# Optimization experiments

Measured on AMD Instinct MI355X. Metric: run time of the kernel, lower is better.

Reference implementation:

```python
import jax, jax.numpy as jnp
import numpy as np

D_MODEL = 1024
N_INPUT = 4096
N_PROCESS = 2048
D_ROUTING = 256
TEMPERATURE = 0.5
LN_EPS = 1e-5


def _gelu(x):
    return jax.nn.gelu(x, approximate=False)  # torch F.gelu default (erf)


def setup_inputs() -> dict:
    key = jax.random.key(0)
    ks = jax.random.split(key, 10)
    B, S = 8, 2048
    x = jax.random.normal(ks[0], (B, S, D_MODEL), dtype=jnp.float32)
    # GlobalRouter query_net: Linear(d_model, 2*d_routing) -> GELU -> LayerNorm -> Linear(2*d_routing, d_routing)
    W1 = jax.random.normal(ks[1], (2 * D_ROUTING, D_MODEL), dtype=jnp.float32) * (2.0 / (D_MODEL + 2 * D_ROUTING)) ** 0.5 * 1.414
    b1 = jnp.zeros((2 * D_ROUTING,), dtype=jnp.float32)
    ln_g = jnp.ones((2 * D_ROUTING,), dtype=jnp.float32)
    ln_b = jnp.zeros((2 * D_ROUTING,), dtype=jnp.float32)
    W2 = jax.random.normal(ks[2], (D_ROUTING, 2 * D_ROUTING), dtype=jnp.float32) * (2.0 / (3 * D_ROUTING)) ** 0.5 * 1.414
    b2 = jnp.zeros((D_ROUTING,), dtype=jnp.float32)
    neuron_keys = jax.random.normal(ks[3], (N_INPUT, D_ROUTING), dtype=jnp.float32) / D_ROUTING ** 0.5 * 1.414
    input_patterns = jax.random.normal(ks[4], (N_INPUT, D_MODEL), dtype=jnp.float32) / D_MODEL ** 0.5 * 1.414
    process_weights = jax.random.normal(ks[5], (N_PROCESS, N_INPUT), dtype=jnp.float32) / N_INPUT ** 0.5 * 1.414
    process_outputs = jax.random.normal(ks[6], (N_PROCESS, D_MODEL), dtype=jnp.float32) / D_MODEL ** 0.5 * 1.414
    return {
        'x': x, 'k_input': 2048, 'k_process': 1024,
        'W1': W1, 'b1': b1, 'ln_g': ln_g, 'ln_b': ln_b, 'W2': W2, 'b2': b2,
        'neuron_keys': neuron_keys, 'input_patterns': input_patterns,
        'process_weights': process_weights, 'process_outputs': process_outputs,
    }


def _forward(x, k_input, k_process, W1, b1, ln_g, ln_b, W2, b2,
             neuron_keys, input_patterns, process_weights, process_outputs):
    B, S, d_model = x.shape
    # ---- GlobalRouter ----
    gctx = jnp.max(x, axis=1)                                  # [B, d_model]
    h = _gelu(gctx @ W1.T + b1)                                # [B, 2*d_routing]
    mu = jnp.mean(h, axis=-1, keepdims=True)
    var = jnp.mean((h - mu) ** 2, axis=-1, keepdims=True)
    h = (h - mu) * jax.lax.rsqrt(var + LN_EPS) * ln_g + ln_b
    query = h @ W2.T + b2                                      # [B, d_routing]
    logits = (query @ neuron_keys.T) / D_ROUTING ** 0.5        # [B, n_input]
    probs = jax.nn.softmax(logits / TEMPERATURE, axis=-1)
    _, input_idx = jax.lax.top_k(logits, k_input)              # [B, k_input]
    one_hot = jnp.zeros_like(probs).at[jnp.arange(B)[:, None], input_idx].set(1.0)
    routing_weights = jax.lax.stop_gradient(one_hot - probs) + probs  # STE
    # ---- input neuron stage ----
    input_acts = _gelu(jnp.einsum('bsd,nd->bsn', x, input_patterns))   # [B,S,n_input]
    weighted = input_acts * routing_weights[:, None, :]
    sel_in = jnp.take_along_axis(weighted, input_idx[:, None, :], axis=2)  # [B,S,k_input]
    # gather process weight columns per batch: [B, n_process, k_input]
    W_sel = jnp.transpose(process_weights[:, input_idx], (1, 0, 2))
    process_acts = _gelu(jnp.einsum('bsk,bpk->bsp', sel_in, W_sel))    # [B,S,n_process]
    # ---- process neuron stage ----
    process_scores = jnp.mean(process_acts, axis=1)                    # [B,n_process]
    _, process_idx = jax.lax.top_k(process_scores, k_process)          # [B,k_process]
    sel_proc = jnp.take_along_axis(process_acts, process_idx[:, None, :], axis=2)  # [B,S,k_process]
    out_sel = process_outputs[process_idx]                             # [B,k_process,d_model]
    return jnp.einsum('bsp,bpd->bsd', sel_proc, out_sel)


def reference(x, k_input, k_process, W1, b1, ln_g, ln_b, W2, b2,
              neuron_keys, input_patterns, process_weights, process_outputs):
    return _forward(x, k_input, k_process, W1, b1, ln_g, ln_b, W2, b2,
                    neuron_keys, input_patterns, process_weights, process_outputs)
```

## Files before the change

kernel.cpp:

```cpp
#include <hip/hip_runtime.h>
#include <stdint.h>

#define B_  8
#define S_  2048
#define DM  1024
#define NI  4096
#define NP  2048
#define DR  256
#define H2  512
#define KI  2048
#define KP  1024
#define LDW 40

typedef __attribute__((ext_vector_type(8))) short bf16x8;
typedef __attribute__((ext_vector_type(4))) float f32x4;
typedef unsigned short ushort;
typedef unsigned int uint;

__device__ __forceinline__ float gelu_erf(float v){
    return 0.5f * v * (1.0f + erff(v * 0.7071067811865476f));
}
__device__ __forceinline__ ushort f2b(float f){
    union { float f; uint u; } a; a.f = f;
    uint r = a.u + 0x7fffu + ((a.u >> 16) & 1u);
    return (ushort)(r >> 16);
}
__device__ __forceinline__ float b2f(ushort u){
    union { uint u; float f; } a; a.u = ((uint)u) << 16; return a.f;
}
__device__ __forceinline__ void cvt8(const float* p, uint4& H, uint4& L){
    uint h[4], l[4];
    #pragma unroll
    for(int i = 0; i < 4; i++){
        ushort h0 = f2b(p[2*i]);   float f0 = b2f(h0); ushort l0 = f2b(p[2*i]   - f0);
        ushort h1 = f2b(p[2*i+1]); float f1 = b2f(h1); ushort l1 = f2b(p[2*i+1] - f1);
        h[i] = (uint)h0 | ((uint)h1 << 16);
        l[i] = (uint)l0 | ((uint)l1 << 16);
    }
    H = uint4{h[0],h[1],h[2],h[3]};
    L = uint4{l[0],l[1],l[2],l[3]};
}
__device__ __forceinline__ void gload_lds16(const void* g, void* l){
    __builtin_amdgcn_global_load_lds((const __attribute__((address_space(1))) void*)g,
                                     (__attribute__((address_space(3))) void*)l, 16, 0, 0);
}

__global__ __launch_bounds__(256) void k_pre(const float* __restrict__ x,
                                             const float* __restrict__ patt,
                                             const float* __restrict__ pout,
                                             float* __restrict__ gpart,
                                             ushort* __restrict__ xh,
                                             ushort* __restrict__ xl,
                                             ushort* __restrict__ patth,
                                             ushort* __restrict__ pattl,
                                             ushort* __restrict__ poutb){
    int bid = blockIdx.x;
    int t = threadIdx.x;
    if(bid < 512){
        int b = bid >> 6, ch = bid & 63;
        size_t row0 = (size_t)b*S_ + (size_t)ch*32;
        const float4* xb = (const float4*)(x + row0*DM);
        float4 m = float4{-3.402823466e38f, -3.402823466e38f, -3.402823466e38f, -3.402823466e38f};
        for(int r = 0; r < 32; r++){
            float4 v = xb[(size_t)r*(DM/4) + t];
            ushort hx = f2b(v.x), hy = f2b(v.y), hz = f2b(v.z), hw = f2b(v.w);
            uint2 H{ (uint)hx | ((uint)hy << 16), (uint)hz | ((uint)hw << 16) };
            uint2 L{ (uint)f2b(v.x - b2f(hx)) | ((uint)f2b(v.y - b2f(hy)) << 16),
                     (uint)f2b(v.z - b2f(hz)) | ((uint)f2b(v.w - b2f(hw)) << 16) };
            ((uint2*)(xh + (row0 + r)*DM))[t] = H;
            ((uint2*)(xl + (row0 + r)*DM))[t] = L;
            m.x = fmaxf(m.x, v.x); m.y = fmaxf(m.y, v.y);
            m.z = fmaxf(m.z, v.z); m.w = fmaxf(m.w, v.w);
        }
        ((float4*)(gpart + (size_t)(b*64 + ch)*DM))[t] = m;
    }else if(bid < 2560){
        size_t idx = (size_t)(bid - 512)*256 + t;
        float f[8];
        *(float4*)(f)     = ((const float4*)patt)[idx*2];
        *(float4*)(f + 4) = ((const float4*)patt)[idx*2 + 1];
        uint4 H, L; cvt8(f, H, L);
        ((uint4*)patth)[idx] = H;
        ((uint4*)pattl)[idx] = L;
    }else{
        size_t idx = (size_t)(bid - 2560)*256 + t;
        float f[8];
        *(float4*)(f)     = ((const float4*)pout)[idx*2];
        *(float4*)(f + 4) = ((const float4*)pout)[idx*2 + 1];
        uint o[4];
        #pragma unroll
        for(int i = 0; i < 4; i++)
            o[i] = (uint)f2b(f[2*i]) | ((uint)f2b(f[2*i+1]) << 16);
        ((uint4*)poutb)[idx] = uint4{o[0], o[1], o[2], o[3]};
    }
}

__global__ __launch_bounds__(256) void k_h(const float* __restrict__ gpart,
                                           const float* __restrict__ W1,
                                           const float* __restrict__ b1,
                                           float* __restrict__ h){
    __shared__ float g[DM];
    int b = blockIdx.x >> 3, ig = blockIdx.x & 7;
    int t = threadIdx.x;
    for(int d = t; d < DM; d += 256){
        float m = gpart[(size_t)(b*64)*DM + d];
        for(int c = 1; c < 64; c++) m = fmaxf(m, gpart[(size_t)(b*64 + c)*DM + d]);
        g[d] = m;
    }
    __syncthreads();
    int i  = ig*64 + (t >> 2);
    int dq = (t & 3) * 256;
    const float* wr = W1 + (size_t)i*DM + dq;
    const float* gg = g + dq;
    float s = 0.f;
    for(int d = 0; d < 256; d++) s = fmaf(gg[d], wr[d], s);
    s += __shfl_xor(s, 1);
    s += __shfl_xor(s, 2);
    if((t & 3) == 0) h[b*H2 + i] = gelu_erf(s + b1[i]);
}

__global__ __launch_bounds__(256) void k_query(const float* __restrict__ h,
                                               const float* __restrict__ lng,
                                               const float* __restrict__ lnb,
                                               const float* __restrict__ W2,
                                               const float* __restrict__ b2,
                                               float* __restrict__ query){
    __shared__ float hn[H2];
    __shared__ float red[4];
    int b = blockIdx.x >> 2, qg = blockIdx.x & 3;
    int t = threadIdx.x;
    float v0 = h[b*H2 + t], v1 = h[b*H2 + 256 + t];
    float s = v0 + v1;
    for(int o = 32; o > 0; o >>= 1) s += __shfl_down(s, o);
    if((t & 63) == 0) red[t >> 6] = s;
    __syncthreads();
    float mean = (red[0] + red[1] + red[2] + red[3]) * (1.f/H2);
    __syncthreads();
    float d0 = v0 - mean, d1 = v1 - mean;
    float sq = d0*d0 + d1*d1;
    for(int o = 32; o > 0; o >>= 1) sq += __shfl_down(sq, o);
    if((t & 63) == 0) red[t >> 6] = sq;
    __syncthreads();
    float var  = (red[0] + red[1] + red[2] + red[3]) * (1.f/H2);
    float rstd = rsqrtf(var + 1e-5f);
    hn[t]       = d0*rstd*lng[t]       + lnb[t];
    hn[256 + t] = d1*rstd*lng[256 + t] + lnb[256 + t];
    __syncthreads();
    int q  = qg*64 + (t >> 2);
    int iq = (t & 3) * 128;
    const float* wr = W2 + (size_t)q*H2 + iq;
    float acc = 0.f;
    for(int i2 = 0; i2 < 128; i2++) acc = fmaf(hn[iq + i2], wr[i2], acc);
    acc += __shfl_xor(acc, 1);
    acc += __shfl_xor(acc, 2);
    if((t & 3) == 0) query[b*DR + q] = acc + b2[q];
}

__global__ __launch_bounds__(256) void k_logits(const float* __restrict__ query,
                                                const float* __restrict__ nk,
                                                float* __restrict__ logits){
    __shared__ float4 q4[DR/4];
    int b = blockIdx.x >> 4, ng = blockIdx.x & 15;
    int t = threadIdx.x;
    if(t < 64) q4[t] = ((const float4*)(query + (size_t)b*DR))[t];
    __syncthreads();
    int w = t >> 6, lane = t & 63;
    float4 qv = q4[lane];
    int nbase = ng*256 + w*64;
    #pragma unroll 2
    for(int i = 0; i < 64; i++){
        int n = nbase + i;
        float4 v = ((const float4*)(nk + (size_t)n*DR))[lane];
        float p = v.x*qv.x + v.y*qv.y + v.z*qv.z + v.w*qv.w;
        p += __shfl_down(p, 32); p += __shfl_down(p, 16); p += __shfl_down(p, 8);
        p += __shfl_down(p, 4);  p += __shfl_down(p, 2);  p += __shfl_down(p, 1);
        if(lane == 0) logits[(size_t)b*NI + n] = p * 0.0625f;
    }
}

template<int N_, int KSEL>
__global__ __launch_bounds__(256) void k_topk(const float* __restrict__ vals,
                                              int* __restrict__ idxout){
    __shared__ unsigned u[N_];
    __shared__ int redc[4];
    __shared__ int sc[256];
    int t = threadIdx.x;
    size_t vbase = (size_t)blockIdx.x * N_;
    size_t obase = (size_t)blockIdx.x * KSEL;
    for(int i = t; i < N_; i += 256){
        unsigned bits = __float_as_uint(vals[vbase + i]);
        u[i] = (bits & 0x80000000u) ? ~bits : (bits | 0x80000000u);
    }
    __syncthreads();
    unsigned lo = 0u, hi = 0xFFFFFFFFu;
    while(lo < hi){
        unsigned mid = lo + (unsigned)((((unsigned long long)(hi - lo)) + 1ull) >> 1);
        int c = 0;
        for(int i = t; i < N_; i += 256) c += (u[i] >= mid) ? 1 : 0;
        for(int o = 32; o > 0; o >>= 1) c += __shfl_down(c, o);
        if((t & 63) == 0) redc[t >> 6] = c;
        __syncthreads();
        int tot = redc[0] + redc[1] + redc[2] + redc[3];
        if(tot >= KSEL) lo = mid; else hi = mid - 1;
        __syncthreads();
    }
    unsigned T = lo;
    const int PER = N_ / 256;
    int base = t * PER;
    int lgt = 0, leq = 0;
    for(int j = 0; j < PER; j++){
        unsigned v = u[base + j];
        lgt += (v > T) ? 1 : 0; leq += (v == T) ? 1 : 0;
    }
    sc[t] = (lgt << 16) | leq;
    __syncthreads();
    for(int o = 1; o < 256; o <<= 1){
        int add = (t >= o) ? sc[t - o] : 0;
        __syncthreads();
        sc[t] += add;
        __syncthreads();
    }
    int need = KSEL - (sc[255] >> 16);
    int ex = (t == 0) ? 0 : sc[t - 1];
    int pos = (ex >> 16) + ((ex & 0xffff) < need ? (ex & 0xffff) : need);
    int eq = ex & 0xffff;
    for(int j = 0; j < PER; j++){
        unsigned v = u[base + j];
        if(v > T){ idxout[obase + pos++] = base + j; }
        else if(v == T){ if(eq < need){ idxout[obase + pos++] = base + j; } eq++; }
    }
}

__global__ __launch_bounds__(256) void k_gemm1(const ushort* __restrict__ xh,
                                               const ushort* __restrict__ xl,
                                               const ushort* __restrict__ ph,
                                               const ushort* __restrict__ pl,
                                               const int* __restrict__ iidx,
                                               ushort* __restrict__ selh,
                                               ushort* __restrict__ sell, int b0){
    __shared__ __align__(16) ushort Ah[2][128*32], Al[2][128*32], Bh[2][128*32], Bl[2][128*32];
    __shared__ int rowmap[128];
    int t = threadIdx.x;
    int g = blockIdx.x >> 8, rest = blockIdx.x & 255;
    int b = b0 + g;
    int mb = rest >> 4, nb = rest & 15;
    int m0 = mb*128, n0 = nb*128;
    ushort* selh_g = selh + (size_t)g*S_*KI;
    ushort* sell_g = sell + (size_t)g*S_*KI;
    if(t < 128) rowmap[t] = iidx[(size_t)b*KI + n0 + t];
    __syncthreads();
    int w = t >> 6, l = t & 63;
    int lr = l >> 2, lc = l & 3;
    int r0 = 32*w + lr, r1 = r0 + 16;
    const ushort* pAh0 = xh + ((size_t)b*S_ + m0 + r0)*DM + lc*8;
    const ushort* pAh1 = xh + ((size_t)b*S_ + m0 + r1)*DM + lc*8;
    const ushort* pAl0 = xl + ((size_t)b*S_ + m0 + r0)*DM + lc*8;
    const ushort* pAl1 = xl + ((size_t)b*S_ + m0 + r1)*DM + lc*8;
    const ushort* pBh0 = ph + (size_t)rowmap[r0]*DM + lc*8;
    const ushort* pBh1 = ph + (size_t)rowmap[r1]*DM + lc*8;
    const ushort* pBl0 = pl + (size_t)rowmap[r0]*DM + lc*8;
    const ushort* pBl1 = pl + (size_t)rowmap[r1]*DM + lc*8;
    int d0 = w*1024, d1 = d0 + 512;
    #define STG1(BUF, KO) do{ \
        gload_lds16(pAh0 + (KO), &Ah[BUF][d0]); \
        gload_lds16(pAh1 + (KO), &Ah[BUF][d1]); \
        gload_lds16(pAl0 + (KO), &Al[BUF][d0]); \
        gload_lds16(pAl1 + (KO), &Al[BUF][d1]); \
        gload_lds16(pBh0 + (KO), &Bh[BUF][d0]); \
        gload_lds16(pBh1 + (KO), &Bh[BUF][d1]); \
        gload_lds16(pBl0 + (KO), &Bl[BUF][d0]); \
        gload_lds16(pBl1 + (KO), &Bl[BUF][d1]); \
    }while(0)
    STG1(0, 0);
    int lm = l & 15, q = l >> 4;
    int mbase = (w >> 1)*64, nbase = (w & 1)*64;
    f32x4 acc[4][4];
    #pragma unroll
    for(int i = 0; i < 4; i++)
      #pragma unroll
      for(int j = 0; j < 4; j++) acc[i][j] = f32x4{0.f,0.f,0.f,0.f};
    int cur = 0;
    for(int k0 = 0; k0 < DM; k0 += 32){
        if(k0 + 32 < DM){
            STG1(cur^1, k0 + 32);
            asm volatile("s_waitcnt vmcnt(8)" ::: "memory");
        }else{
            asm volatile("s_waitcnt vmcnt(0)" ::: "memory");
        }
        __builtin_amdgcn_s_barrier();
        asm volatile("" ::: "memory");
        bf16x8 ahf[4], alf[4];
        #pragma unroll
        for(int mt = 0; mt < 4; mt++){
            ahf[mt] = *(const bf16x8*)(&Ah[cur][(mbase + mt*16 + lm)*32 + q*8]);
            alf[mt] = *(const bf16x8*)(&Al[cur][(mbase + mt*16 + lm)*32 + q*8]);
        }
        __builtin_amdgcn_s_setprio(1);
        #pragma unroll
        for(int nt = 0; nt < 4; nt++){
            bf16x8 bhf = *(const bf16x8*)(&Bh[cur][(nbase + nt*16 + lm)*32 + q*8]);
            bf16x8 blf = *(const bf16x8*)(&Bl[cur][(nbase + nt*16 + lm)*32 + q*8]);
            #pragma unroll
            for(int mt = 0; mt < 4; mt++){
                acc[mt][nt] = __builtin_amdgcn_mfma_f32_16x16x32_bf16(ahf[mt], bhf, acc[mt][nt], 0, 0, 0);
                acc[mt][nt] = __builtin_amdgcn_mfma_f32_16x16x32_bf16(ahf[mt], blf, acc[mt][nt], 0, 0, 0);
                acc[mt][nt] = __builtin_amdgcn_mfma_f32_16x16x32_bf16(alf[mt], bhf, acc[mt][nt], 0, 0, 0);
            }
        }
        __builtin_amdgcn_s_setprio(0);
        asm volatile("s_waitcnt lgkmcnt(0)" ::: "memory");
        __builtin_amdgcn_s_barrier();
        asm volatile("" ::: "memory");
        cur ^= 1;
    }
    #undef STG1
    #pragma unroll
    for(int mt = 0; mt < 4; mt++)
      #pragma unroll
      for(int nt = 0; nt < 4; nt++){
        int col = n0 + nbase + nt*16 + lm;
        #pragma unroll
        for(int i = 0; i < 4; i++){
            int row = m0 + mbase + mt*16 + q*4 + i;
            float gv = gelu_erf(acc[mt][nt][i]);
            ushort hbits = f2b(gv);
            selh_g[(size_t)row*KI + col] = hbits;
            sell_g[(size_t)row*KI + col] = f2b(gv - b2f(hbits));
        }
      }
}

__global__ __launch_bounds__(256) void k_gather_wsel(const float* __restrict__ pw,
                                                     const int* __restrict__ iidx,
                                                     ushort* __restrict__ wh,
                                                     ushort* __restrict__ wl,
                                                     float* __restrict__ scores, int b0){
    int g = blockIdx.x >> 8, pc = blockIdx.x & 255;
    int b = b0 + g;
    ushort* wh_g = wh + (size_t)g*NP*KI;
    ushort* wl_g = wl + (size_t)g*NP*KI;
    int t = threadIdx.x;
    if(t < 8) scores[(size_t)b*NP + pc*8 + t] = 0.f;
    int j0 = t*8;
    int k8[8];
    *(int4*)(k8)     = *(const int4*)(iidx + (size_t)b*KI + j0);
    *(int4*)(k8 + 4) = *(const int4*)(iidx + (size_t)b*KI + j0 + 4);
    for(int r2 = 0; r2 < 8; r2++){
        int p = pc*8 + r2;
        const float* row = pw + (size_t)p*NI;
        uint hh[4], ll[4];
        #pragma unroll
        for(int i = 0; i < 4; i++){
            float v0 = row[k8[2*i]], v1 = row[k8[2*i+1]];
            ushort h0 = f2b(v0), h1 = f2b(v1);
            hh[i] = (uint)h0 | ((uint)h1 << 16);
            ll[i] = (uint)f2b(v0 - b2f(h0)) | ((uint)f2b(v1 - b2f(h1)) << 16);
        }
        *(uint4*)(wh_g + (size_t)p*KI + j0) = uint4{hh[0],hh[1],hh[2],hh[3]};
        *(uint4*)(wl_g + (size_t)p*KI + j0) = uint4{ll[0],ll[1],ll[2],ll[3]};
    }
}

__global__ __launch_bounds__(256) void k_gemm2(const ushort* __restrict__ selh,
                                               const ushort* __restrict__ sell,
                                               const ushort* __restrict__ wh,
                                               const ushort* __restrict__ wl,
                                               ushort* __restrict__ acts,
                                               float* __restrict__ scores, int b0){
    __shared__ __align__(16) ushort Ah[2][128*32], Al[2][128*32], Bh[2][128*32], Bl[2][128*32];
    __shared__ float colsum[128];
    int t = threadIdx.x;
    int g = blockIdx.x >> 8, rest = blockIdx.x & 255;
    int b = b0 + g;
    int mb = rest >> 4, nb = rest & 15;
    int m0 = mb*128, n0 = nb*128;
    const ushort* selh_g = selh + (size_t)g*S_*KI;
    const ushort* sell_g = sell + (size_t)g*S_*KI;
    const ushort* wh_g   = wh   + (size_t)g*NP*KI;
    const ushort* wl_g   = wl   + (size_t)g*NP*KI;
    ushort* acts_g = acts + (size_t)g*S_*NP;
    int w = t >> 6, l = t & 63;
    int lr = l >> 2, lc = l & 3;
    int r0 = 32*w + lr, r1 = r0 + 16;
    const ushort* pAh0 = selh_g + (size_t)(m0 + r0)*KI + lc*8;
    const ushort* pAh1 = selh_g + (size_t)(m0 + r1)*KI + lc*8;
    const ushort* pAl0 = sell_g + (size_t)(m0 + r0)*KI + lc*8;
    const ushort* pAl1 = sell_g + (size_t)(m0 + r1)*KI + lc*8;
    const ushort* pBh0 = wh_g + (size_t)(n0 + r0)*KI + lc*8;
    const ushort* pBh1 = wh_g + (size_t)(n0 + r1)*KI + lc*8;
    const ushort* pBl0 = wl_g + (size_t)(n0 + r0)*KI + lc*8;
    const ushort* pBl1 = wl_g + (size_t)(n0 + r1)*KI + lc*8;
    int d0 = w*1024, d1 = d0 + 512;
    #define STG2(BUF, KO) do{ \
        gload_lds16(pAh0 + (KO), &Ah[BUF][d0]); \
        gload_lds16(pAh1 + (KO), &Ah[BUF][d1]); \
        gload_lds16(pAl0 + (KO), &Al[BUF][d0]); \
        gload_lds16(pAl1 + (KO), &Al[BUF][d1]); \
        gload_lds16(pBh0 + (KO), &Bh[BUF][d0]); \
        gload_lds16(pBh1 + (KO), &Bh[BUF][d1]); \
        gload_lds16(pBl0 + (KO), &Bl[BUF][d0]); \
        gload_lds16(pBl1 + (KO), &Bl[BUF][d1]); \
    }while(0)
    STG2(0, 0);
    int lm = l & 15, q = l >> 4;
    int mbase = (w >> 1)*64, nbase = (w & 1)*64;
    f32x4 acc[4][4];
    #pragma unroll
    for(int i = 0; i < 4; i++)
      #pragma unroll
      for(int j = 0; j < 4; j++) acc[i][j] = f32x4{0.f,0.f,0.f,0.f};
    int cur = 0;
    for(int k0 = 0; k0 < KI; k0 += 32){
        if(k0 + 32 < KI){
            STG2(cur^1, k0 + 32);
            asm volatile("s_waitcnt vmcnt(8)" ::: "memory");
        }else{
            asm volatile("s_waitcnt vmcnt(0)" ::: "memory");
        }
        __builtin_amdgcn_s_barrier();
        asm volatile("" ::: "memory");
        bf16x8 ahf[4], alf[4];
        #pragma unroll
        for(int mt = 0; mt < 4; mt++){
            ahf[mt] = *(const bf16x8*)(&Ah[cur][(mbase + mt*16 + lm)*32 + q*8]);
            alf[mt] = *(const bf16x8*)(&Al[cur][(mbase + mt*16 + lm)*32 + q*8]);
        }
        __builtin_amdgcn_s_setprio(1);
        #pragma unroll
        for(int nt = 0; nt < 4; nt++){
            bf16x8 bhf = *(const bf16x8*)(&Bh[cur][(nbase + nt*16 + lm)*32 + q*8]);
            bf16x8 blf = *(const bf16x8*)(&Bl[cur][(nbase + nt*16 + lm)*32 + q*8]);
            #pragma unroll
            for(int mt = 0; mt < 4; mt++){
                acc[mt][nt] = __builtin_amdgcn_mfma_f32_16x16x32_bf16(ahf[mt], bhf, acc[mt][nt], 0, 0, 0);
                acc[mt][nt] = __builtin_amdgcn_mfma_f32_16x16x32_bf16(ahf[mt], blf, acc[mt][nt], 0, 0, 0);
                acc[mt][nt] = __builtin_amdgcn_mfma_f32_16x16x32_bf16(alf[mt], bhf, acc[mt][nt], 0, 0, 0);
            }
        }
        __builtin_amdgcn_s_setprio(0);
        asm volatile("s_waitcnt lgkmcnt(0)" ::: "memory");
        __builtin_amdgcn_s_barrier();
        asm volatile("" ::: "memory");
        cur ^= 1;
    }
    #undef STG2
    if(t < 128) colsum[t] = 0.f;
    __syncthreads();
    #pragma unroll
    for(int mt = 0; mt < 4; mt++)
      #pragma unroll
      for(int nt = 0; nt < 4; nt++){
        int cb = nbase + nt*16 + lm;
        float s4 = 0.f;
        #pragma unroll
        for(int i = 0; i < 4; i++){
            int row = m0 + mbase + mt*16 + q*4 + i;
            float gv = gelu_erf(acc[mt][nt][i]);
            s4 += gv;
            acts_g[(size_t)row*NP + n0 + cb] = f2b(gv);
        }
        atomicAdd(&colsum[cb], s4);
      }
    __syncthreads();
    if(t < 128) atomicAdd(&scores[(size_t)b*NP + n0 + t], colsum[t]);
}

__global__ __launch_bounds__(256) void k_gather_selacts(const ushort* __restrict__ acts,
                                                        const int* __restrict__ pidx,
                                                        ushort* __restrict__ selacts, int b0){
    int g = blockIdx.x >> 6, sc_ = blockIdx.x & 63;
    int b = b0 + g;
    const ushort* acts_g = acts + (size_t)g*S_*NP;
    ushort* selacts_g = selacts + (size_t)g*S_*KP;
    int t = threadIdx.x;
    int j0 = t*4;
    int4 p4 = *(const int4*)(pidx + (size_t)b*KP + j0);
    const ushort* Ab = acts_g    + ((size_t)sc_*32)*NP;
    ushort*       Ob = selacts_g + ((size_t)sc_*32)*KP;
    for(int r2 = 0; r2 < 32; r2++){
        const ushort* Ar = Ab + (size_t)r2*NP;
        ushort o0 = Ar[p4.x], o1 = Ar[p4.y], o2 = Ar[p4.z], o3 = Ar[p4.w];
        uint2 ov{ (uint)o0 | ((uint)o1 << 16), (uint)o2 | ((uint)o3 << 16) };
        *(uint2*)(Ob + (size_t)r2*KP + j0) = ov;
    }
}

__global__ __launch_bounds__(256) void k_gemm3(const ushort* __restrict__ selacts,
                                               const ushort* __restrict__ poutb,
                                               const int* __restrict__ pidx,
                                               float* __restrict__ out, int b0){
    __shared__ __align__(16) ushort As[2][128*32];
    __shared__ __align__(16) ushort Bs[2][128*LDW];
    __shared__ int pix[KP];
    int t = threadIdx.x;
    int g = blockIdx.x >> 7, rest = blockIdx.x & 127;
    int b = b0 + g;
    int mb = rest >> 3, nb = rest & 7;
    int m0 = mb*128, n0 = nb*128;
    const ushort* sel_g = selacts + (size_t)g*S_*KP;
    int w = t >> 6, l = t & 63;
    int lr = l >> 2, lc = l & 3;
    int r0 = 32*w + lr, r1 = r0 + 16;
    const ushort* pA0 = sel_g + (size_t)(m0 + r0)*KP + lc*8;
    const ushort* pA1 = sel_g + (size_t)(m0 + r1)*KP + lc*8;
    int d0 = w*1024, d1 = d0 + 512;
    gload_lds16(pA0, &As[0][d0]);
    gload_lds16(pA1, &As[0][d1]);
    for(int i = t; i < KP; i += 256) pix[i] = pidx[(size_t)b*KP + i];
    __syncthreads();
    int kk = t >> 3, nc = (t & 7)*16;
    uint4 B0, B1;
    {
        const ushort* bg = poutb + (size_t)pix[kk]*DM + n0 + nc;
        B0 = *(const uint4*)(bg); B1 = *(const uint4*)(bg + 8);
    }
    int lm = l & 15, q = l >> 4;
    int mbase = (w >> 1)*64, nbase = (w & 1)*64;
    f32x4 acc[4][4];
    #pragma unroll
    for(int i = 0; i < 4; i++)
      #pragma unroll
      for(int j = 0; j < 4; j++) acc[i][j] = f32x4{0.f,0.f,0.f,0.f};
    for(int k0 = 0; k0 < KP; k0 += 32){
        int cur = (k0 >> 5) & 1;
        {
            const ushort* pb0 = (const ushort*)&B0;
            const ushort* pb1 = (const ushort*)&B1;
            #pragma unroll
            for(int c = 0; c < 8; c++) Bs[cur][(nc + c)*LDW + kk]     = pb0[c];
            #pragma unroll
            for(int c = 0; c < 8; c++) Bs[cur][(nc + 8 + c)*LDW + kk] = pb1[c];
        }
        if(k0 + 32 < KP){
            gload_lds16(pA0 + (k0 + 32), &As[cur^1][d0]);
            gload_lds16(pA1 + (k0 + 32), &As[cur^1][d1]);
            asm volatile("s_waitcnt vmcnt(2)" ::: "memory");
        }else{
            asm volatile("s_waitcnt vmcnt(0)" ::: "memory");
        }
        asm volatile("s_waitcnt lgkmcnt(0)" ::: "memory");
        __builtin_amdgcn_s_barrier();
        asm volatile("" ::: "memory");
        if(k0 + 32 < KP){
            const ushort* bg = poutb + (size_t)pix[k0 + 32 + kk]*DM + n0 + nc;
            B0 = *(const uint4*)(bg); B1 = *(const uint4*)(bg + 8);
        }
        bf16x8 af[4];
        #pragma unroll
        for(int mt = 0; mt < 4; mt++)
            af[mt] = *(const bf16x8*)(&As[cur][(mbase + mt*16 + lm)*32 + q*8]);
        __builtin_amdgcn_s_setprio(1);
        #pragma unroll
        for(int nt = 0; nt < 4; nt++){
            bf16x8 bf = *(const bf16x8*)(&Bs[cur][(nbase + nt*16 + lm)*LDW + q*8]);
            #pragma unroll
            for(int mt = 0; mt < 4; mt++)
                acc[mt][nt] = __builtin_amdgcn_mfma_f32_16x16x32_bf16(af[mt], bf, acc[mt][nt], 0, 0, 0);
        }
        __builtin_amdgcn_s_setprio(0);
        asm volatile("s_waitcnt lgkmcnt(0)" ::: "memory");
        __builtin_amdgcn_s_barrier();
        asm volatile("" ::: "memory");
    }
    float* Cb = out + (size_t)b*S_*DM;
    #pragma unroll
    for(int mt = 0; mt < 4; mt++)
      #pragma unroll
      for(int nt = 0; nt < 4; nt++){
        int col = n0 + nbase + nt*16 + lm;
        #pragma unroll
        for(int i = 0; i < 4; i++){
            int row = m0 + mbase + mt*16 + q*4 + i;
            Cb[(size_t)row*DM + col] = acc[mt][nt][i];
        }
      }
}

extern "C" void kernel_launch(void* const* d_in, const int* in_sizes, int n_in,
                              void* d_out, int out_size, void* d_ws, size_t ws_size,
                              hipStream_t stream){
    const float* x    = (const float*)d_in[0];
    const float* W1   = (const float*)d_in[3];
    const float* b1   = (const float*)d_in[4];
    const float* lng  = (const float*)d_in[5];
    const float* lnb  = (const float*)d_in[6];
    const float* W2   = (const float*)d_in[7];
    const float* b2   = (const float*)d_in[8];
    const float* nk   = (const float*)d_in[9];
    const float* patt = (const float*)d_in[10];
    const float* pw   = (const float*)d_in[11];
    const float* pout = (const float*)d_in[12];
    float* out = (float*)d_out;

    auto al256 = [](size_t v){ return (v + 255) & ~(size_t)255; };
    const size_t fixed =
        al256((size_t)B_*64*DM*4) + al256((size_t)B_*H2*4) + al256((size_t)B_*DR*4) +
        al256((size_t)B_*NI*4)    + al256((size_t)B_*KI*4) + al256((size_t)B_*NP*4) +
        al256((size_t)B_*KP*4) +
        2*al256((size_t)B_*S_*DM*2) + 2*al256((size_t)NI*DM*2) + al256((size_t)NP*DM*2);
    const size_t perb = (size_t)S_*KI*2*2 + (size_t)NP*KI*2*2 + (size_t)S_*NP*2 + (size_t)S_*KP*2 + 6*256;
    int G = 8;
    while(G > 1 && fixed + (size_t)G*perb > ws_size) G >>= 1;
    if(fixed + (size_t)G*perb > ws_size) return;

    char* wsp = (char*)d_ws;
    size_t off = 0;
    auto alloc = [&](size_t bytes) -> void* {
        void* p = wsp + off;
        off += (bytes + 255) & ~(size_t)255;
        return p;
    };
    float*  gpart   = (float*) alloc((size_t)B_*64*DM*4);
    float*  h       = (float*) alloc((size_t)B_*H2*4);
    float*  query   = (float*) alloc((size_t)B_*DR*4);
    float*  logits  = (float*) alloc((size_t)B_*NI*4);
    int*    iidx    = (int*)   alloc((size_t)B_*KI*4);
    float*  scores  = (float*) alloc((size_t)B_*NP*4);
    int*    pidx    = (int*)   alloc((size_t)B_*KP*4);
    ushort* xh      = (ushort*)alloc((size_t)B_*S_*DM*2);
    ushort* xl      = (ushort*)alloc((size_t)B_*S_*DM*2);
    ushort* patth   = (ushort*)alloc((size_t)NI*DM*2);
    ushort* pattl   = (ushort*)alloc((size_t)NI*DM*2);
    ushort* poutb   = (ushort*)alloc((size_t)NP*DM*2);
    ushort* selh    = (ushort*)alloc((size_t)G*S_*KI*2);
    ushort* sell    = (ushort*)alloc((size_t)G*S_*KI*2);
    ushort* wselh   = (ushort*)alloc((size_t)G*NP*KI*2);
    ushort* wsell   = (ushort*)alloc((size_t)G*NP*KI*2);
    ushort* acts    = (ushort*)alloc((size_t)G*S_*NP*2);
    ushort* selacts = (ushort*)alloc((size_t)G*S_*KP*2);

    dim3 blk(256);
    k_pre   <<<3584, blk, 0, stream>>>(x, patt, pout, gpart, xh, xl, patth, pattl, poutb);
    k_h     <<<64,  blk, 0, stream>>>(gpart, W1, b1, h);
    k_query <<<32,  blk, 0, stream>>>(h, lng, lnb, W2, b2, query);
    k_logits<<<128, blk, 0, stream>>>(query, nk, logits);
    k_topk<NI, KI><<<B_, blk, 0, stream>>>(logits, iidx);
    for(int b0 = 0; b0 < B_; b0 += G){
        k_gemm1        <<<G*256, blk, 0, stream>>>(xh, xl, patth, pattl, iidx, selh, sell, b0);
        k_gather_wsel  <<<G*256, blk, 0, stream>>>(pw, iidx, wselh, wsell, scores, b0);
        k_gemm2        <<<G*256, blk, 0, stream>>>(selh, sell, wselh, wsell, acts, scores, b0);
        k_topk<NP, KP> <<<G,     blk, 0, stream>>>(scores + (size_t)b0*NP, pidx + (size_t)b0*KP);
        k_gather_selacts<<<G*64, blk, 0, stream>>>(acts, pidx, selacts, b0);
        k_gemm3        <<<G*128, blk, 0, stream>>>(selacts, poutb, pidx, out, b0);
    }
}
```

Baseline: 1.344 ms.

## Replace binary-search top-k with 4-pass radix select and retune small kernels

The top-k kernel's 32-step binary search over threshold values is replaced by a byte-wise radix select: four histogram passes with shared-memory atomics and suffix scans. Blocks grow to 1024 threads to cut per-thread serial work. The max-reduction chunking in k_pre is doubled to 64 rows per block, halving gpart partials and the work in k_h. k_logits launches twice as many blocks. The goal is to shorten the serial, latency-bound router stages, at the cost of atomic contention in the histogram passes.

```diff
diff --git a/kernel.cpp b/kernel.cpp
--- a/kernel.cpp
+++ b/kernel.cpp
@@ -56,12 +56,12 @@
                                              ushort* __restrict__ poutb){
     int bid = blockIdx.x;
     int t = threadIdx.x;
-    if(bid < 512){
-        int b = bid >> 6, ch = bid & 63;
-        size_t row0 = (size_t)b*S_ + (size_t)ch*32;
+    if(bid < 256){
+        int b = bid >> 5, ch = bid & 31;
+        size_t row0 = (size_t)b*S_ + (size_t)ch*64;
         const float4* xb = (const float4*)(x + row0*DM);
         float4 m = float4{-3.402823466e38f, -3.402823466e38f, -3.402823466e38f, -3.402823466e38f};
-        for(int r = 0; r < 32; r++){
+        for(int r = 0; r < 64; r++){
             float4 v = xb[(size_t)r*(DM/4) + t];
             ushort hx = f2b(v.x), hy = f2b(v.y), hz = f2b(v.z), hw = f2b(v.w);
             uint2 H{ (uint)hx | ((uint)hy << 16), (uint)hz | ((uint)hw << 16) };
@@ -72,9 +72,9 @@
             m.x = fmaxf(m.x, v.x); m.y = fmaxf(m.y, v.y);
             m.z = fmaxf(m.z, v.z); m.w = fmaxf(m.w, v.w);
         }
-        ((float4*)(gpart + (size_t)(b*64 + ch)*DM))[t] = m;
-    }else if(bid < 2560){
-        size_t idx = (size_t)(bid - 512)*256 + t;
+        ((float4*)(gpart + (size_t)(b*32 + ch)*DM))[t] = m;
+    }else if(bid < 2304){
+        size_t idx = (size_t)(bid - 256)*256 + t;
         float f[8];
         *(float4*)(f)     = ((const float4*)patt)[idx*2];
         *(float4*)(f + 4) = ((const float4*)patt)[idx*2 + 1];
@@ -82,7 +82,7 @@
         ((uint4*)patth)[idx] = H;
         ((uint4*)pattl)[idx] = L;
     }else{
-        size_t idx = (size_t)(bid - 2560)*256 + t;
+        size_t idx = (size_t)(bid - 2304)*256 + t;
         float f[8];
         *(float4*)(f)     = ((const float4*)pout)[idx*2];
         *(float4*)(f + 4) = ((const float4*)pout)[idx*2 + 1];
@@ -102,8 +102,8 @@
     int b = blockIdx.x >> 3, ig = blockIdx.x & 7;
     int t = threadIdx.x;
     for(int d = t; d < DM; d += 256){
-        float m = gpart[(size_t)(b*64)*DM + d];
-        for(int c = 1; c < 64; c++) m = fmaxf(m, gpart[(size_t)(b*64 + c)*DM + d]);
+        float m = gpart[(size_t)(b*32)*DM + d];
+        for(int c = 1; c < 32; c++) m = fmaxf(m, gpart[(size_t)(b*32 + c)*DM + d]);
         g[d] = m;
     }
     __syncthreads();
@@ -159,15 +159,15 @@
                                                 const float* __restrict__ nk,
                                                 float* __restrict__ logits){
     __shared__ float4 q4[DR/4];
-    int b = blockIdx.x >> 4, ng = blockIdx.x & 15;
+    int b = blockIdx.x >> 5, ng = blockIdx.x & 31;
     int t = threadIdx.x;
     if(t < 64) q4[t] = ((const float4*)(query + (size_t)b*DR))[t];
     __syncthreads();
     int w = t >> 6, lane = t & 63;
     float4 qv = q4[lane];
-    int nbase = ng*256 + w*64;
+    int nbase = ng*128 + w*32;
     #pragma unroll 2
-    for(int i = 0; i < 64; i++){
+    for(int i = 0; i < 32; i++){
         int n = nbase + i;
         float4 v = ((const float4*)(nk + (size_t)n*DR))[lane];
         float p = v.x*qv.x + v.y*qv.y + v.z*qv.z + v.w*qv.w;
@@ -178,33 +178,51 @@
 }
 
 template<int N_, int KSEL>
-__global__ __launch_bounds__(256) void k_topk(const float* __restrict__ vals,
-                                              int* __restrict__ idxout){
+__global__ __launch_bounds__(1024) void k_topk(const float* __restrict__ vals,
+                                               int* __restrict__ idxout){
     __shared__ unsigned u[N_];
-    __shared__ int redc[4];
-    __shared__ int sc[256];
+    __shared__ int hist[256];
+    __shared__ int sfx[512];
+    __shared__ int sc[1024];
+    __shared__ int sel_d, sel_need;
     int t = threadIdx.x;
     size_t vbase = (size_t)blockIdx.x * N_;
     size_t obase = (size_t)blockIdx.x * KSEL;
-    for(int i = t; i < N_; i += 256){
+    for(int i = t; i < N_; i += 1024){
         unsigned bits = __float_as_uint(vals[vbase + i]);
         u[i] = (bits & 0x80000000u) ? ~bits : (bits | 0x80000000u);
     }
-    __syncthreads();
-    unsigned lo = 0u, hi = 0xFFFFFFFFu;
-    while(lo < hi){
-        unsigned mid = lo + (unsigned)((((unsigned long long)(hi - lo)) + 1ull) >> 1);
-        int c = 0;
-        for(int i = t; i < N_; i += 256) c += (u[i] >= mid) ? 1 : 0;
-        for(int o = 32; o > 0; o >>= 1) c += __shfl_down(c, o);
-        if((t & 63) == 0) redc[t >> 6] = c;
+    unsigned long long prefix = 0;
+    int need = KSEL;
+    for(int bb = 3; bb >= 0; bb--){
+        if(t < 256) hist[t] = 0;
         __syncthreads();
-        int tot = redc[0] + redc[1] + redc[2] + redc[3];
-        if(tot >= KSEL) lo = mid; else hi = mid - 1;
+        for(int i = t; i < N_; i += 1024){
+            unsigned v = u[i];
+            if(((unsigned long long)v >> ((bb + 1)*8)) == prefix)
+                atomicAdd(&hist[(v >> (bb*8)) & 255], 1);
+        }
         __syncthreads();
-    }
-    unsigned T = lo;
-    const int PER = N_ / 256;
+        if(t < 256) sfx[t] = hist[t];
+        else if(t < 512) sfx[t] = 0;
+        __syncthreads();
+        for(int o = 1; o < 256; o <<= 1){
+            int v2 = (t < 256) ? sfx[t + o] : 0;
+            __syncthreads();
+            if(t < 256) sfx[t] += v2;
+            __syncthreads();
+        }
+        if(t < 256){
+            int hi_c = sfx[t + 1];
+            if(sfx[t] >= need && hi_c < need){ sel_d = t; sel_need = need - hi_c; }
+        }
+        __syncthreads();
+        prefix = (prefix << 8) | (unsigned)sel_d;
+        need = sel_need;
+        __syncthreads();
+    }
+    unsigned T = (unsigned)prefix;
+    const int PER = N_ / 1024;
     int base = t * PER;
     int lgt = 0, leq = 0;
     for(int j = 0; j < PER; j++){
@@ -213,20 +231,20 @@
     }
     sc[t] = (lgt << 16) | leq;
     __syncthreads();
-    for(int o = 1; o < 256; o <<= 1){
+    for(int o = 1; o < 1024; o <<= 1){
         int add = (t >= o) ? sc[t - o] : 0;
         __syncthreads();
         sc[t] += add;
         __syncthreads();
     }
-    int need = KSEL - (sc[255] >> 16);
+    int need2 = KSEL - (sc[1023] >> 16);
     int ex = (t == 0) ? 0 : sc[t - 1];
-    int pos = (ex >> 16) + ((ex & 0xffff) < need ? (ex & 0xffff) : need);
+    int pos = (ex >> 16) + ((ex & 0xffff) < need2 ? (ex & 0xffff) : need2);
     int eq = ex & 0xffff;
     for(int j = 0; j < PER; j++){
         unsigned v = u[base + j];
         if(v > T){ idxout[obase + pos++] = base + j; }
-        else if(v == T){ if(eq < need){ idxout[obase + pos++] = base + j; } eq++; }
+        else if(v == T){ if(eq < need2){ idxout[obase + pos++] = base + j; } eq++; }
     }
 }
 
@@ -593,7 +611,7 @@
 
     auto al256 = [](size_t v){ return (v + 255) & ~(size_t)255; };
     const size_t fixed =
-        al256((size_t)B_*64*DM*4) + al256((size_t)B_*H2*4) + al256((size_t)B_*DR*4) +
+        al256((size_t)B_*32*DM*4) + al256((size_t)B_*H2*4) + al256((size_t)B_*DR*4) +
         al256((size_t)B_*NI*4)    + al256((size_t)B_*KI*4) + al256((size_t)B_*NP*4) +
         al256((size_t)B_*KP*4) +
         2*al256((size_t)B_*S_*DM*2) + 2*al256((size_t)NI*DM*2) + al256((size_t)NP*DM*2);
@@ -609,7 +627,7 @@
         off += (bytes + 255) & ~(size_t)255;
         return p;
     };
-    float*  gpart   = (float*) alloc((size_t)B_*64*DM*4);
+    float*  gpart   = (float*) alloc((size_t)B_*32*DM*4);
     float*  h       = (float*) alloc((size_t)B_*H2*4);
     float*  query   = (float*) alloc((size_t)B_*DR*4);
     float*  logits  = (float*) alloc((size_t)B_*NI*4);
@@ -629,16 +647,16 @@
     ushort* selacts = (ushort*)alloc((size_t)G*S_*KP*2);
 
     dim3 blk(256);
-    k_pre   <<<3584, blk, 0, stream>>>(x, patt, pout, gpart, xh, xl, patth, pattl, poutb);
+    k_pre   <<<3328, blk, 0, stream>>>(x, patt, pout, gpart, xh, xl, patth, pattl, poutb);
     k_h     <<<64,  blk, 0, stream>>>(gpart, W1, b1, h);
     k_query <<<32,  blk, 0, stream>>>(h, lng, lnb, W2, b2, query);
-    k_logits<<<128, blk, 0, stream>>>(query, nk, logits);
-    k_topk<NI, KI><<<B_, blk, 0, stream>>>(logits, iidx);
+    k_logits<<<B_*32, blk, 0, stream>>>(query, nk, logits);
+    k_topk<NI, KI><<<B_, dim3(1024), 0, stream>>>(logits, iidx);
     for(int b0 = 0; b0 < B_; b0 += G){
         k_gemm1        <<<G*256, blk, 0, stream>>>(xh, xl, patth, pattl, iidx, selh, sell, b0);
         k_gather_wsel  <<<G*256, blk, 0, stream>>>(pw, iidx, wselh, wsell, scores, b0);
         k_gemm2        <<<G*256, blk, 0, stream>>>(selh, sell, wselh, wsell, acts, scores, b0);
-        k_topk<NP, KP> <<<G,     blk, 0, stream>>>(scores + (size_t)b0*NP, pidx + (size_t)b0*KP);
+        k_topk<NP, KP> <<<G,     dim3(1024), 0, stream>>>(scores + (size_t)b0*NP, pidx + (size_t)b0*KP);
         k_gather_selacts<<<G*64, blk, 0, stream>>>(acts, pidx, selacts, b0);
         k_gemm3        <<<G*128, blk, 0, stream>>>(selacts, poutb, pidx, out, b0);
     }
```

After: 1.334 ms. No clear change (-0.8%).
